# Kernel optimization log

Hardware: AMD Instinct MI355X
Metric: run time of the kernel (lower is better)

Reference implementation:

```python
import jax, jax.numpy as jnp
import numpy as np

RBF_START = 0.0
RBF_END = 10.0
RBF_STEPS = 64
OUT_SIZE = 64
ENERGY_SCALE = 0.1
P, L, R = 8, 128, 1024
COORD_SCALE = 5.0  # spread coords so pair distances span the 0-10 RBF range


def setup_inputs() -> dict:
    key = jax.random.key(0)
    k1, k2, k3, k4 = jax.random.split(key, 4)
    return {
        "lig_feat": jax.random.normal(k1, (L, RBF_STEPS, OUT_SIZE), dtype=jnp.float32),
        "rec_feat": jax.random.normal(k2, (R, RBF_STEPS, OUT_SIZE), dtype=jnp.float32),
        "lig_coords": jax.random.normal(k3, (P, L, 3), dtype=jnp.float32) * COORD_SCALE,
        "rec_coords": jax.random.normal(k4, (R, 3), dtype=jnp.float32) * COORD_SCALE,
    }


def reference(lig_feat, rec_feat, lig_coords, rec_coords):
    # attention coefficients: contract feature axis f -> [L, R, E]
    atn_coefs = jnp.einsum("lef,ref->lre", lig_feat, rec_feat)
    # pairwise distances for every pose: [P, L, R]
    diff = lig_coords[:, :, None, :] - rec_coords[None, None, :, :]
    dists = jnp.sqrt(jnp.sum(diff * diff, axis=-1))
    # RBF expansion: [P, L, R, E]
    mu = jnp.linspace(RBF_START, RBF_END, RBF_STEPS, dtype=jnp.float32)
    sigma = (RBF_START - RBF_END) / RBF_STEPS
    rbfs = jnp.exp(-(((dists[..., None] - mu) / sigma) ** 2))
    # attention-weighted energy per pose: [P]
    Us = jnp.einsum("plre,lre->p", rbfs, atn_coefs) * ENERGY_SCALE
    return Us
```

## Files before the change

kernel.cpp:

```cpp
#include <hip/hip_runtime.h>
#include <math.h>

#define Lc 128
#define Rc 1024
#define Pc 8
#define Ec 64
#define Fc 64

#define CSCALE   7.68718341623328f
#define MU_STEP  0.15873015873015873f
#define MUC      (MU_STEP * CSCALE)

#define BM 32
#define BN 32
#define EC 8
#define NBLKM ((Lc/BM)*(Rc/BN)*(Ec/EC))

typedef __attribute__((ext_vector_type(8))) short short8;
typedef __attribute__((ext_vector_type(4))) float f32x4;

__device__ __forceinline__ unsigned short bf16_rn(float x) {
    unsigned int u = __float_as_uint(x);
    u += 0x7FFF + ((u >> 16) & 1);
    return (unsigned short)(u >> 16);
}
__device__ __forceinline__ unsigned int hipack(float x0, float x1) {
    return (__float_as_uint(x0) >> 16) | (__float_as_uint(x1) & 0xFFFF0000u);
}
__device__ __forceinline__ unsigned int lopack(float x0, float x1) {
    float r0 = x0 - __uint_as_float(__float_as_uint(x0) & 0xFFFF0000u);
    float r1 = x1 - __uint_as_float(__float_as_uint(x1) & 0xFFFF0000u);
    return ((unsigned int)bf16_rn(r1) << 16) | (unsigned int)bf16_rn(r0);
}

__global__ __launch_bounds__(256, 2)
void ff_mfma(const float* __restrict__ lig_feat,
             const float* __restrict__ rec_feat,
             const float* __restrict__ lig_coords,
             const float* __restrict__ rec_coords,
             float* __restrict__ partial)
{
    __shared__ __align__(16) unsigned short stg[2][2][32][16][8];
    __shared__ float lcs[Pc][96];
    __shared__ float rcs[96];
    __shared__ float wred[4][Pc];

    const int tid  = threadIdx.x;
    const int lane = tid & 63;
    const int w    = tid >> 6;
    const int n16  = lane & 15;
    const int kg   = lane >> 4;
    const int sr   = w >> 1;
    const int sc   = w & 1;

    const int bid = blockIdx.x;
    const int loc = bid >> 3;
    const int rt  = (bid & 7) * 4 + (loc & 3);
    const int lt  = (loc >> 2) & 3;
    const int ez  = loc >> 4;
    const int r0  = rt * BN;
    const int l0  = lt * BM;
    const int e0  = ez * EC;

    for (int i = tid; i < Pc * 96; i += 256) {
        int p = i / 96, q = i - p * 96;
        lcs[p][q] = lig_coords[p * (Lc * 3) + l0 * 3 + q];
    }
    if (tid < 96) rcs[tid] = rec_coords[r0 * 3 + tid];
    __syncthreads();

    float dsc[Pc][4];
    {
        const int rb = (sc * 16 + n16) * 3;
        const float rx = rcs[rb], ry = rcs[rb + 1], rz = rcs[rb + 2];
        #pragma unroll
        for (int reg = 0; reg < 4; ++reg) {
            const int lb = (sr * 16 + kg * 4 + reg) * 3;
            #pragma unroll
            for (int p = 0; p < Pc; ++p) {
                float dx = lcs[p][lb]     - rx;
                float dy = lcs[p][lb + 1] - ry;
                float dz = lcs[p][lb + 2] - rz;
                dsc[p][reg] = sqrtf(dx * dx + dy * dy + dz * dz) * CSCALE;
            }
        }
    }

    const int half = tid >> 7;
    const int srow = (tid >> 2) & 31;
    const int fq   = tid & 3;
    const float* sbase = (half ? rec_feat + (size_t)(r0 + srow) * (Ec * Fc)
                               : lig_feat + (size_t)(l0 + srow) * (Ec * Fc)) + fq * 16;

    float4 pf[4];
    auto ld = [&](int e) {
        #pragma unroll
        for (int j = 0; j < 4; ++j)
            pf[j] = *(const float4*)(sbase + (size_t)e * Fc + j * 4);
    };
    auto cw = [&](int nb) {
        uint4 H0, H1, L0, L1;
        H0.x = hipack(pf[0].x, pf[0].y); H0.y = hipack(pf[0].z, pf[0].w);
        H0.z = hipack(pf[1].x, pf[1].y); H0.w = hipack(pf[1].z, pf[1].w);
        H1.x = hipack(pf[2].x, pf[2].y); H1.y = hipack(pf[2].z, pf[2].w);
        H1.z = hipack(pf[3].x, pf[3].y); H1.w = hipack(pf[3].z, pf[3].w);
        L0.x = lopack(pf[0].x, pf[0].y); L0.y = lopack(pf[0].z, pf[0].w);
        L0.z = lopack(pf[1].x, pf[1].y); L0.w = lopack(pf[1].z, pf[1].w);
        L1.x = lopack(pf[2].x, pf[2].y); L1.y = lopack(pf[2].z, pf[2].w);
        L1.z = lopack(pf[3].x, pf[3].y); L1.w = lopack(pf[3].z, pf[3].w);
        const int sm = srow & 15;
        *(uint4*)&stg[nb][half][srow][(fq * 2)         ^ sm][0] = H0;
        *(uint4*)&stg[nb][half][srow][(fq * 2 + 1)     ^ sm][0] = H1;
        *(uint4*)&stg[nb][half][srow][(8 + fq * 2)     ^ sm][0] = L0;
        *(uint4*)&stg[nb][half][srow][(8 + fq * 2 + 1) ^ sm][0] = L1;
    };

    ld(e0);
    cw(0);
    ld(e0 + 1);
    asm volatile("s_waitcnt lgkmcnt(0)" ::: "memory");
    __builtin_amdgcn_sched_barrier(0);
    __builtin_amdgcn_s_barrier();
    __builtin_amdgcn_sched_barrier(0);

    float us[Pc];
    #pragma unroll
    for (int p = 0; p < Pc; ++p) us[p] = 0.f;

    const int Arow = sr * 16 + n16;
    const int Brow = sc * 16 + n16;
#define RD(hf, rowv, slot) (*(const short8*)&stg[cur][hf][rowv][(slot) ^ ((rowv) & 15)][0])

    for (int t = 0; t < EC; ++t) {
        const int cur = t & 1;

        f32x4 acc = {0.f, 0.f, 0.f, 0.f};
        {
            short8 a0 = RD(0, Arow, kg);
            short8 b0 = RD(1, Brow, kg);
            acc = __builtin_amdgcn_mfma_f32_16x16x32_bf16(a0, b0, acc, 0, 0, 0);
            short8 a1 = RD(0, Arow, 8 + kg);
            acc = __builtin_amdgcn_mfma_f32_16x16x32_bf16(a1, b0, acc, 0, 0, 0);
            short8 b1 = RD(1, Brow, 8 + kg);
            acc = __builtin_amdgcn_mfma_f32_16x16x32_bf16(a0, b1, acc, 0, 0, 0);
            a0 = RD(0, Arow, 4 + kg);
            b0 = RD(1, Brow, 4 + kg);
            acc = __builtin_amdgcn_mfma_f32_16x16x32_bf16(a0, b0, acc, 0, 0, 0);
            a1 = RD(0, Arow, 12 + kg);
            acc = __builtin_amdgcn_mfma_f32_16x16x32_bf16(a1, b0, acc, 0, 0, 0);
            b1 = RD(1, Brow, 12 + kg);
            acc = __builtin_amdgcn_mfma_f32_16x16x32_bf16(a0, b1, acc, 0, 0, 0);
        }

        if (t + 1 < EC) {
            cw((t + 1) & 1);
            if (t + 2 < EC) ld(e0 + t + 2);
            asm volatile("s_waitcnt lgkmcnt(0)" ::: "memory");
            __builtin_amdgcn_sched_barrier(0);
            __builtin_amdgcn_s_barrier();
            __builtin_amdgcn_sched_barrier(0);
        }

        const float musC = (float)(e0 + t) * MUC;
        #pragma unroll
        for (int reg = 0; reg < 4; ++reg) {
            const float av = acc[reg];
            #pragma unroll
            for (int p = 0; p < Pc; ++p) {
                const float tt = dsc[p][reg] - musC;
                us[p] = fmaf(av, __builtin_amdgcn_exp2f(-tt * tt), us[p]);
            }
        }
    }
#undef RD

    #pragma unroll
    for (int p = 0; p < Pc; ++p) {
        float v = us[p];
        #pragma unroll
        for (int off = 32; off >= 1; off >>= 1)
            v += __shfl_xor(v, off, 64);
        us[p] = v;
    }
    if (lane == 0) {
        #pragma unroll
        for (int p = 0; p < Pc; ++p) wred[w][p] = us[p];
    }
    __syncthreads();
    if (tid < Pc) {
        float s = 0.f;
        #pragma unroll
        for (int k = 0; k < 4; ++k) s += wred[k][tid];
        partial[(size_t)bid * Pc + tid] = s;
    }
}

__global__ void ff_reduce(const float* __restrict__ partial, float* __restrict__ out)
{
    const int w    = threadIdx.x >> 6;
    const int lane = threadIdx.x & 63;
    float v = 0.f;
    #pragma unroll
    for (int j = 0; j < NBLKM / 64; ++j)
        v += partial[(size_t)(lane + 64 * j) * Pc + w];
    #pragma unroll
    for (int off = 32; off >= 1; off >>= 1)
        v += __shfl_xor(v, off, 64);
    if (lane == 0) out[w] = 0.1f * v;
}

extern "C" void kernel_launch(void* const* d_in, const int* in_sizes, int n_in,
                              void* d_out, int out_size, void* d_ws, size_t ws_size,
                              hipStream_t stream)
{
    const float* lig_feat   = (const float*)d_in[0];
    const float* rec_feat   = (const float*)d_in[1];
    const float* lig_coords = (const float*)d_in[2];
    const float* rec_coords = (const float*)d_in[3];
    float* out     = (float*)d_out;
    float* partial = (float*)d_ws;

    ff_mfma<<<NBLKM, 256, 0, stream>>>(lig_feat, rec_feat, lig_coords, rec_coords, partial);
    ff_reduce<<<1, 512, 0, stream>>>(partial, out);
}
```

Before: 34.12 us.

## Use 512-thread blocks splitting E-chunk across two wave groups sharing coords

Each block now covers 16 E-steps split between two independent groups of 4 waves, each with its own double-buffered LDS staging. This halves the block count and shares the coordinate and distance setup across twice the work. The first feature global load is also issued before the coordinate staging so the two overlap. The partial-sum layout becomes pose-major so the final reduce reads contiguously. The cost is more LDS per block and larger blocks under a 2-block-per-CU launch bound, which may raise register pressure.

```diff
diff --git a/kernel.cpp b/kernel.cpp
--- a/kernel.cpp
+++ b/kernel.cpp
@@ -13,8 +13,9 @@
 
 #define BM 32
 #define BN 32
-#define EC 8
-#define NBLKM ((Lc/BM)*(Rc/BN)*(Ec/EC))
+#define ECB 16
+#define EH 8
+#define NBLKM ((Lc/BM) * (Rc/BN) * (Ec/ECB))
 
 typedef __attribute__((ext_vector_type(8))) short short8;
 typedef __attribute__((ext_vector_type(4))) float f32x4;
@@ -33,25 +34,27 @@
     return ((unsigned int)bf16_rn(r1) << 16) | (unsigned int)bf16_rn(r0);
 }
 
-__global__ __launch_bounds__(256, 2)
+__global__ __launch_bounds__(512, 2)
 void ff_mfma(const float* __restrict__ lig_feat,
              const float* __restrict__ rec_feat,
              const float* __restrict__ lig_coords,
              const float* __restrict__ rec_coords,
              float* __restrict__ partial)
 {
-    __shared__ __align__(16) unsigned short stg[2][2][32][16][8];
+    __shared__ __align__(16) unsigned short stg[2][2][2][32][16][8];
     __shared__ float lcs[Pc][96];
     __shared__ float rcs[96];
-    __shared__ float wred[4][Pc];
+    __shared__ float wred[8][Pc];
 
     const int tid  = threadIdx.x;
     const int lane = tid & 63;
     const int w    = tid >> 6;
+    const int se   = w >> 2;
+    const int wq   = w & 3;
     const int n16  = lane & 15;
     const int kg   = lane >> 4;
-    const int sr   = w >> 1;
-    const int sc   = w & 1;
+    const int sr   = wq >> 1;
+    const int sc   = wq & 1;
 
     const int bid = blockIdx.x;
     const int loc = bid >> 3;
@@ -60,37 +63,13 @@
     const int ez  = loc >> 4;
     const int r0  = rt * BN;
     const int l0  = lt * BM;
-    const int e0  = ez * EC;
-
-    for (int i = tid; i < Pc * 96; i += 256) {
-        int p = i / 96, q = i - p * 96;
-        lcs[p][q] = lig_coords[p * (Lc * 3) + l0 * 3 + q];
-    }
-    if (tid < 96) rcs[tid] = rec_coords[r0 * 3 + tid];
-    __syncthreads();
-
-    float dsc[Pc][4];
-    {
-        const int rb = (sc * 16 + n16) * 3;
-        const float rx = rcs[rb], ry = rcs[rb + 1], rz = rcs[rb + 2];
-        #pragma unroll
-        for (int reg = 0; reg < 4; ++reg) {
-            const int lb = (sr * 16 + kg * 4 + reg) * 3;
-            #pragma unroll
-            for (int p = 0; p < Pc; ++p) {
-                float dx = lcs[p][lb]     - rx;
-                float dy = lcs[p][lb + 1] - ry;
-                float dz = lcs[p][lb + 2] - rz;
-                dsc[p][reg] = sqrtf(dx * dx + dy * dy + dz * dz) * CSCALE;
-            }
-        }
-    }
-
-    const int half = tid >> 7;
+    const int eh  = ez * ECB + se * EH;
+
+    const int sgA  = (tid >> 7) & 1;
     const int srow = (tid >> 2) & 31;
     const int fq   = tid & 3;
-    const float* sbase = (half ? rec_feat + (size_t)(r0 + srow) * (Ec * Fc)
-                               : lig_feat + (size_t)(l0 + srow) * (Ec * Fc)) + fq * 16;
+    const float* sbase = (sgA ? rec_feat + (size_t)(r0 + srow) * (Ec * Fc)
+                              : lig_feat + (size_t)(l0 + srow) * (Ec * Fc)) + fq * 16;
 
     float4 pf[4];
     auto ld = [&](int e) {
@@ -109,15 +88,40 @@
         L1.x = lopack(pf[2].x, pf[2].y); L1.y = lopack(pf[2].z, pf[2].w);
         L1.z = lopack(pf[3].x, pf[3].y); L1.w = lopack(pf[3].z, pf[3].w);
         const int sm = srow & 15;
-        *(uint4*)&stg[nb][half][srow][(fq * 2)         ^ sm][0] = H0;
-        *(uint4*)&stg[nb][half][srow][(fq * 2 + 1)     ^ sm][0] = H1;
-        *(uint4*)&stg[nb][half][srow][(8 + fq * 2)     ^ sm][0] = L0;
-        *(uint4*)&stg[nb][half][srow][(8 + fq * 2 + 1) ^ sm][0] = L1;
+        *(uint4*)&stg[se][nb][sgA][srow][(fq * 2)         ^ sm][0] = H0;
+        *(uint4*)&stg[se][nb][sgA][srow][(fq * 2 + 1)     ^ sm][0] = H1;
+        *(uint4*)&stg[se][nb][sgA][srow][(8 + fq * 2)     ^ sm][0] = L0;
+        *(uint4*)&stg[se][nb][sgA][srow][(8 + fq * 2 + 1) ^ sm][0] = L1;
     };
 
-    ld(e0);
+    ld(eh);
+
+    for (int i = tid; i < Pc * 96; i += 512) {
+        int p = i / 96, q = i - p * 96;
+        lcs[p][q] = lig_coords[p * (Lc * 3) + l0 * 3 + q];
+    }
+    if (tid < 96) rcs[tid] = rec_coords[r0 * 3 + tid];
+    __syncthreads();
+
+    float dsc[Pc][4];
+    {
+        const int rb = (sc * 16 + n16) * 3;
+        const float rx = rcs[rb], ry = rcs[rb + 1], rz = rcs[rb + 2];
+        #pragma unroll
+        for (int reg = 0; reg < 4; ++reg) {
+            const int lb = (sr * 16 + kg * 4 + reg) * 3;
+            #pragma unroll
+            for (int p = 0; p < Pc; ++p) {
+                float dx = lcs[p][lb]     - rx;
+                float dy = lcs[p][lb + 1] - ry;
+                float dz = lcs[p][lb + 2] - rz;
+                dsc[p][reg] = sqrtf(dx * dx + dy * dy + dz * dz) * CSCALE;
+            }
+        }
+    }
+
     cw(0);
-    ld(e0 + 1);
+    ld(eh + 1);
     asm volatile("s_waitcnt lgkmcnt(0)" ::: "memory");
     __builtin_amdgcn_sched_barrier(0);
     __builtin_amdgcn_s_barrier();
@@ -129,9 +133,9 @@
 
     const int Arow = sr * 16 + n16;
     const int Brow = sc * 16 + n16;
-#define RD(hf, rowv, slot) (*(const short8*)&stg[cur][hf][rowv][(slot) ^ ((rowv) & 15)][0])
-
-    for (int t = 0; t < EC; ++t) {
+#define RD(hf, rowv, slot) (*(const short8*)&stg[se][cur][hf][rowv][(slot) ^ ((rowv) & 15)][0])
+
+    for (int t = 0; t < EH; ++t) {
         const int cur = t & 1;
 
         f32x4 acc = {0.f, 0.f, 0.f, 0.f};
@@ -152,16 +156,16 @@
             acc = __builtin_amdgcn_mfma_f32_16x16x32_bf16(a0, b1, acc, 0, 0, 0);
         }
 
-        if (t + 1 < EC) {
+        if (t + 1 < EH) {
             cw((t + 1) & 1);
-            if (t + 2 < EC) ld(e0 + t + 2);
+            if (t + 2 < EH) ld(eh + t + 2);
             asm volatile("s_waitcnt lgkmcnt(0)" ::: "memory");
             __builtin_amdgcn_sched_barrier(0);
             __builtin_amdgcn_s_barrier();
             __builtin_amdgcn_sched_barrier(0);
         }
 
-        const float musC = (float)(e0 + t) * MUC;
+        const float musC = (float)(eh + t) * MUC;
         #pragma unroll
         for (int reg = 0; reg < 4; ++reg) {
             const float av = acc[reg];
@@ -190,8 +194,8 @@
     if (tid < Pc) {
         float s = 0.f;
         #pragma unroll
-        for (int k = 0; k < 4; ++k) s += wred[k][tid];
-        partial[(size_t)bid * Pc + tid] = s;
+        for (int k = 0; k < 8; ++k) s += wred[k][tid];
+        partial[(size_t)tid * NBLKM + bid] = s;
     }
 }
 
@@ -202,7 +206,7 @@
     float v = 0.f;
     #pragma unroll
     for (int j = 0; j < NBLKM / 64; ++j)
-        v += partial[(size_t)(lane + 64 * j) * Pc + w];
+        v += partial[(size_t)w * NBLKM + lane + 64 * j];
     #pragma unroll
     for (int off = 32; off >= 1; off >>= 1)
         v += __shfl_xor(v, off, 64);
@@ -220,6 +224,6 @@
     float* out     = (float*)d_out;
     float* partial = (float*)d_ws;
 
-    ff_mfma<<<NBLKM, 256, 0, stream>>>(lig_feat, rec_feat, lig_coords, rec_coords, partial);
+    ff_mfma<<<NBLKM, 512, 0, stream>>>(lig_feat, rec_feat, lig_coords, rec_coords, partial);
     ff_reduce<<<1, 512, 0, stream>>>(partial, out);
 }
```

Measured after the change: 32.09 us. 1.06x faster.
